# Performance work log

Measured on AMD Instinct MI355X. Metric: run time of the kernel, lower is better.

Reference implementation:

```python
import jax, jax.numpy as jnp
import numpy as np

EPS = 1e-12

def l2_normalize(x, axis=-1):
    # matches torch F.normalize(p=2, dim=1, eps=1e-12) for 2D input
    n = jnp.sqrt(jnp.sum(x * x, axis=axis, keepdims=True))
    return x / jnp.maximum(n, EPS)

def setup_inputs() -> dict:
    key = jax.random.key(0)
    ks = jax.random.split(key, 7)
    N, D = 8192, 256
    s = 1.0 / np.sqrt(D)
    x = jax.random.normal(ks[0], (N, D), dtype=jnp.float32)
    Wq = jax.random.uniform(ks[1], (D, D), jnp.float32, -s, s)
    bq = jax.random.uniform(ks[2], (D,), jnp.float32, -s, s)
    Wk = jax.random.uniform(ks[3], (D, D), jnp.float32, -s, s)
    bk = jax.random.uniform(ks[4], (D,), jnp.float32, -s, s)
    Wv = jax.random.uniform(ks[5], (D, D), jnp.float32, -s, s)
    bv = jax.random.uniform(ks[6], (D,), jnp.float32, -s, s)
    return {"x": x, "Wq": Wq, "bq": bq, "Wk": Wk, "bk": bk, "Wv": Wv, "bv": bv}

def reference(x, Wq, bq, Wk, bk, Wv, bv):
    q = l2_normalize(x @ Wq.T + bq)           # [N, D]
    k = l2_normalize(x @ Wk.T + bk)           # [N, D]
    v = x @ Wv.T + bv                         # [N, D]
    cos_sim = q @ k.T                         # [N, N]
    w = jax.nn.relu(cos_sim)
    # zero diagonal, then renormalize rows to sum 1
    N = w.shape[0]
    w = jnp.where(jnp.eye(N, dtype=bool), 0.0, w)
    w = w / jnp.maximum(jnp.sum(w, axis=-1, keepdims=True), EPS)
    return w @ v + x
```

## Files before the change

kernel.cpp:

```cpp
#include <hip/hip_runtime.h>

#define NROWS 8192
#define DDIM  256
#define KSPLIT 4
#define BM 128
#define BK 64
#define NT (NROWS / KSPLIT / BK)

typedef __bf16 bf16x8 __attribute__((ext_vector_type(8)));
typedef float  f32x4  __attribute__((ext_vector_type(4)));
typedef float  f32x16 __attribute__((ext_vector_type(16)));

typedef __attribute__((address_space(1))) unsigned int uint_gas;
typedef __attribute__((address_space(3))) unsigned int uint_las;

__device__ __forceinline__ void gload_lds16(const void* g, void* l) {
  __builtin_amdgcn_global_load_lds((const uint_gas*)g, (uint_las*)l, 16, 0, 0);
}

__device__ __forceinline__ unsigned int f2bf_bits(float f) {
  union { float f; unsigned int u; } v; v.f = f;
  unsigned int r = v.u + 0x7FFFu + ((v.u >> 16) & 1u);
  return r >> 16;
}
__device__ __forceinline__ float bf2f(unsigned int b) {
  union { unsigned int u; float f; } v; v.u = b << 16;
  return v.f;
}
__device__ __forceinline__ unsigned int pack2bf(float a, float b) {
  union { unsigned int u; __bf16 h[2]; } p;
  p.h[0] = (__bf16)a; p.h[1] = (__bf16)b;
  return p.u;
}
__device__ __forceinline__ unsigned short f2h_bits(float f) {
  union { _Float16 h; unsigned short u; } c; c.h = (_Float16)f;
  return c.u;
}
__device__ __forceinline__ float h2f(unsigned short u) {
  union { unsigned short u; _Float16 h; } c; c.u = u;
  return (float)c.h;
}

#define NXFRAG (512 * 8 * 64)
#define NWFRAG (3 * 16 * 8 * 64)
__global__ __launch_bounds__(256) void convert_kernel(
    const float* __restrict__ x, const float* __restrict__ wq,
    const float* __restrict__ wk, const float* __restrict__ wv,
    unsigned short* __restrict__ xp, unsigned short* __restrict__ Wp)
{
  int tid = blockIdx.x * 256 + threadIdx.x;
  const float* src;
  unsigned short* dst;
  int row, col;
  if (tid < NXFRAG) {
    int l = tid & 63, ks = (tid >> 6) & 7, rt = tid >> 9;
    src = x; dst = xp + (size_t)tid * 8;
    row = rt * 16 + (l & 15); col = ks * 32 + (l >> 4) * 8;
  } else {
    int fid = tid - NXFRAG;
    if (fid >= NWFRAG) return;
    int l = fid & 63, ks = (fid >> 6) & 7, ct = (fid >> 9) & 15, out = fid >> 13;
    src = (out == 0) ? wq : (out == 1) ? wk : wv;
    dst = Wp + (size_t)fid * 8;
    row = ct * 16 + (l & 15); col = ks * 32 + (l >> 4) * 8;
  }
  const float* p = src + (size_t)row * DDIM + col;
  float4 f0 = *(const float4*)p;
  float4 f1 = *(const float4*)(p + 4);
  ushort4 o0, o1;
  o0.x = (unsigned short)f2bf_bits(f0.x); o0.y = (unsigned short)f2bf_bits(f0.y);
  o0.z = (unsigned short)f2bf_bits(f0.z); o0.w = (unsigned short)f2bf_bits(f0.w);
  o1.x = (unsigned short)f2bf_bits(f1.x); o1.y = (unsigned short)f2bf_bits(f1.y);
  o1.z = (unsigned short)f2bf_bits(f1.z); o1.w = (unsigned short)f2bf_bits(f1.w);
  *(ushort4*)dst = o0;
  *(ushort4*)(dst + 4) = o1;
}

__global__ __launch_bounds__(256) void qkv_kernel(
    const float* __restrict__ bq, const float* __restrict__ bk, const float* __restrict__ bv,
    const unsigned short* __restrict__ xp, const unsigned short* __restrict__ Wp,
    unsigned short* __restrict__ qb, unsigned short* __restrict__ kb,
    unsigned short* __restrict__ vT)
{
  __shared__ unsigned short vstage[DDIM * 72];
  const int t = threadIdx.x;
  const int w = t >> 6, l = t & 63;
  const int c = l & 15, g = l >> 4;
  const int out = blockIdx.x / 128;
  const int mb  = blockIdx.x % 128;
  const int row0 = mb * 64;
  const int rw = row0 + w * 16;
  const int rt = mb * 4 + w;

  bf16x8 a[8];
  #pragma unroll
  for (int ks = 0; ks < 8; ks++)
    a[ks] = *(const bf16x8*)(xp + ((size_t)(rt * 8 + ks) * 64 + l) * 8);

  const float* bias = (out == 0) ? bq : (out == 1) ? bk : bv;
  f32x4 vals[16];
  #pragma unroll
  for (int ct = 0; ct < 16; ct++) {
    f32x4 acc = {0.f, 0.f, 0.f, 0.f};
    #pragma unroll
    for (int ks = 0; ks < 8; ks++) {
      bf16x8 b = *(const bf16x8*)(Wp + ((size_t)((out * 16 + ct) * 8 + ks) * 64 + l) * 8);
      acc = __builtin_amdgcn_mfma_f32_16x16x32_bf16(a[ks], b, acc, 0, 0, 0);
    }
    float bias_v = bias[ct * 16 + c];
    #pragma unroll
    for (int r = 0; r < 4; r++) acc[r] += bias_v;
    vals[ct] = acc;
  }
  if (out < 2) {
    #pragma unroll
    for (int r = 0; r < 4; r++) {
      float ss = 0.f;
      #pragma unroll
      for (int ct = 0; ct < 16; ct++) ss += vals[ct][r] * vals[ct][r];
      ss += __shfl_xor(ss, 1); ss += __shfl_xor(ss, 2);
      ss += __shfl_xor(ss, 4); ss += __shfl_xor(ss, 8);
      float inv = 1.f / fmaxf(sqrtf(ss), 1e-12f);
      #pragma unroll
      for (int ct = 0; ct < 16; ct++) vals[ct][r] *= inv;
    }
    unsigned short* dst = (out == 0) ? qb : kb;
    #pragma unroll
    for (int ct = 0; ct < 16; ct++) {
      #pragma unroll
      for (int r = 0; r < 4; r++) {
        unsigned int bits = f2bf_bits(vals[ct][r]);
        unsigned int ob = (unsigned int)__shfl_xor((int)bits, 1);
        if (!(l & 1))
          *(unsigned int*)(dst + (size_t)(rw + g * 4 + r) * DDIM + ct * 16 + c) =
              bits | (ob << 16);
      }
    }
  } else {
    #pragma unroll
    for (int ct = 0; ct < 16; ct++)
      #pragma unroll
      for (int r = 0; r < 4; r++)
        vstage[(ct * 16 + c) * 72 + (w * 16 + g * 4 + r)] =
            (unsigned short)f2bf_bits(vals[ct][r]);
    __syncthreads();
    #pragma unroll
    for (int p = 0; p < 8; p++) {
      int dd = (t >> 3) + p * 32;
      int ch = t & 7;
      *(uint4*)(vT + (size_t)dd * NROWS + row0 + ch * 8) =
          *(const uint4*)(vstage + dd * 72 + ch * 8);
    }
  }
}

__global__ __launch_bounds__(1024, 4) void attn_kernel(
    const unsigned short* __restrict__ qb, const unsigned short* __restrict__ kb,
    const unsigned short* __restrict__ vT,
    unsigned short* __restrict__ nump, float* __restrict__ denp)
{
  __shared__ __align__(16) char smem[163840];
  char* kbuf = smem;
  char* vbuf = smem + 65536;
  char* Pb   = smem + 131072;

  const int t = threadIdx.x;
  const int w = t >> 6, l = t & 63;
  const int l31 = l & 31, hi = l >> 5;
  const int rw = w & 7;
  const int ts = t & 511;
  const int bid = blockIdx.x;
  const int split = bid & (KSPLIT - 1);
  const int mb = bid >> 2;
  const int q0 = mb * BM;
  const int kbase0 = split * (NROWS / KSPLIT);
  const char* kbc = (const char*)kb;
  const char* vtc = (const char*)vT;

  if (w < 8) {
    const int sr = rw >> 1, sc = rw & 1;
    const int qrow = sr * 32 + l31;
    const int qrowg = q0 + qrow;
    const int krl = sc * 32 + l31;
    const int pswz = (qrow & 7) << 4;

    bf16x8 qa[16];
    {
      const unsigned short* qrowp = qb + (size_t)(q0 + qrow) * DDIM + hi * 8;
      #pragma unroll
      for (int m = 0; m < 16; m++) qa[m] = *(const bf16x8*)(qrowp + m * 16);
    }
    float denl = 0.f;

    auto stageK = [&](int buf, int it) {
      const char* ksrc = kbc + (size_t)(kbase0 + it * BK) * 512;
      #pragma unroll
      for (int i = 0; i < 4; i++) {
        int n = i * 512 + ts;
        int row = n >> 5, slot = n & 31;
        gload_lds16(ksrc + row * 512 + (((slot - row) & 31) << 4),
                    kbuf + buf * 32768 + i * 8192 + rw * 1024);
      }
    };

    stageK(0, 0);
    asm volatile("s_waitcnt vmcnt(0)" ::: "memory");
    __builtin_amdgcn_sched_barrier(0);
    __builtin_amdgcn_s_barrier();
    __builtin_amdgcn_sched_barrier(0);

    for (int it = 0; it < NT; ++it) {
      const int cur = it & 1;
      if (it + 1 < NT) stageK(cur ^ 1, it + 1);
      __builtin_amdgcn_sched_barrier(0);

      const char* kcur = kbuf + cur * 32768;
      f32x16 sacc = (f32x16){0.f};
      #pragma unroll
      for (int m = 0; m < 16; m++) {
        bf16x8 kf = *(const bf16x8*)(kcur + krl * 512 +
                                     (((m * 2 + hi + krl) & 31) << 4));
        sacc = __builtin_amdgcn_mfma_f32_32x32x16_bf16(kf, qa[m], sacc, 0, 0, 0);
      }
      char* prowP = Pb + cur * 16384 + qrow * 128;
      const int kbase = kbase0 + it * BK;
      if (__builtin_expect(kbase < q0 + BM && q0 < kbase + BK, 0)) {
        const int dref = qrowg - (kbase + sc * 32 + hi * 4);
        #pragma unroll
        for (int q = 0; q < 4; q++) {
          float v0 = fmaxf(sacc[4 * q + 0], 0.f);
          float v1 = fmaxf(sacc[4 * q + 1], 0.f);
          float v2 = fmaxf(sacc[4 * q + 2], 0.f);
          float v3 = fmaxf(sacc[4 * q + 3], 0.f);
          const int d = dref - 8 * q;
          v0 = (d == 0) ? 0.f : v0;
          v1 = (d == 1) ? 0.f : v1;
          v2 = (d == 2) ? 0.f : v2;
          v3 = (d == 3) ? 0.f : v3;
          denl += (v0 + v1) + (v2 + v3);
          uint2 d2;
          d2.x = pack2bf(v0, v1);
          d2.y = pack2bf(v2, v3);
          *(uint2*)(prowP + ((sc * 64 + q * 16 + hi * 8) ^ pswz)) = d2;
        }
      } else {
        #pragma unroll
        for (int q = 0; q < 4; q++) {
          float v0 = fmaxf(sacc[4 * q + 0], 0.f);
          float v1 = fmaxf(sacc[4 * q + 1], 0.f);
          float v2 = fmaxf(sacc[4 * q + 2], 0.f);
          float v3 = fmaxf(sacc[4 * q + 3], 0.f);
          denl += (v0 + v1) + (v2 + v3);
          uint2 d2;
          d2.x = pack2bf(v0, v1);
          d2.y = pack2bf(v2, v3);
          *(uint2*)(prowP + ((sc * 64 + q * 16 + hi * 8) ^ pswz)) = d2;
        }
      }
      asm volatile("s_waitcnt vmcnt(0) lgkmcnt(0)" ::: "memory");
      __builtin_amdgcn_sched_barrier(0);
      __builtin_amdgcn_s_barrier();
      __builtin_amdgcn_sched_barrier(0);
    }

    float d = denl;
    d += __shfl_xor(d, 32);
    if (l < 32)
      denp[((size_t)split * 2 + sc) * NROWS + q0 + sr * 32 + l] = d;
  } else {
    const int pr = rw >> 2, pc = rw & 3;
    const int pr0 = pr * 64 + l31, pr1 = pr * 64 + 32 + l31;

    f32x16 oacc[2][2];
    #pragma unroll
    for (int rt = 0; rt < 2; rt++)
      #pragma unroll
      for (int dt = 0; dt < 2; dt++)
        oacc[rt][dt] = (f32x16){0.f};

    auto stageV = [&](int buf, int it) {
      const char* vsrc = vtc + (size_t)(kbase0 + it * BK) * 2;
      #pragma unroll
      for (int i = 0; i < 4; i++) {
        int n = i * 512 + ts;
        int dd = n >> 3, slot = n & 7;
        gload_lds16(vsrc + (size_t)dd * (NROWS * 2) + ((slot ^ (dd & 7)) * 16),
                    vbuf + buf * 32768 + i * 8192 + rw * 1024);
      }
    };

    __builtin_amdgcn_s_barrier();
    __builtin_amdgcn_sched_barrier(0);

    for (int it = 0; it < NT; ++it) {
      const int cur = it & 1;
      stageV(cur, it);
      __builtin_amdgcn_sched_barrier(0);

      if (it > 0) {
        const char* Pprev = Pb + (cur ^ 1) * 16384;
        const char* vprev = vbuf + (cur ^ 1) * 32768;
        #pragma unroll
        for (int ch = 0; ch < 4; ch++) {
          const int cb = ch * 32 + hi * 16;
          bf16x8 pa0 = *(const bf16x8*)(Pprev + pr0 * 128 + (cb ^ ((pr0 & 7) << 4)));
          bf16x8 pa1 = *(const bf16x8*)(Pprev + pr1 * 128 + (cb ^ ((pr1 & 7) << 4)));
          #pragma unroll
          for (int dt = 0; dt < 2; dt++) {
            int dl = pc * 64 + dt * 32 + l31;
            bf16x8 vf = *(const bf16x8*)(vprev + dl * 128 + (cb ^ ((dl & 7) << 4)));
            oacc[0][dt] = __builtin_amdgcn_mfma_f32_32x32x16_bf16(pa0, vf, oacc[0][dt], 0, 0, 0);
            oacc[1][dt] = __builtin_amdgcn_mfma_f32_32x32x16_bf16(pa1, vf, oacc[1][dt], 0, 0, 0);
          }
        }
      }
      asm volatile("s_waitcnt vmcnt(0) lgkmcnt(0)" ::: "memory");
      __builtin_amdgcn_sched_barrier(0);
      __builtin_amdgcn_s_barrier();
      __builtin_amdgcn_sched_barrier(0);
    }

    {
      const int last = (NT - 1) & 1;
      const char* Pprev = Pb + last * 16384;
      const char* vprev = vbuf + last * 32768;
      #pragma unroll
      for (int ch = 0; ch < 4; ch++) {
        const int cb = ch * 32 + hi * 16;
        bf16x8 pa0 = *(const bf16x8*)(Pprev + pr0 * 128 + (cb ^ ((pr0 & 7) << 4)));
        bf16x8 pa1 = *(const bf16x8*)(Pprev + pr1 * 128 + (cb ^ ((pr1 & 7) << 4)));
        #pragma unroll
        for (int dt = 0; dt < 2; dt++) {
          int dl = pc * 64 + dt * 32 + l31;
          bf16x8 vf = *(const bf16x8*)(vprev + dl * 128 + (cb ^ ((dl & 7) << 4)));
          oacc[0][dt] = __builtin_amdgcn_mfma_f32_32x32x16_bf16(pa0, vf, oacc[0][dt], 0, 0, 0);
          oacc[1][dt] = __builtin_amdgcn_mfma_f32_32x32x16_bf16(pa1, vf, oacc[1][dt], 0, 0, 0);
        }
      }
    }

    unsigned short* np = nump + (size_t)split * NROWS * DDIM;
    #pragma unroll
    for (int rt = 0; rt < 2; rt++)
      #pragma unroll
      for (int dt = 0; dt < 2; dt++)
        #pragma unroll
        for (int r = 0; r < 16; r++) {
          int rowg = q0 + pr * 64 + rt * 32 + (r & 3) + 8 * (r >> 2) + 4 * hi;
          int col  = pc * 64 + dt * 32 + l31;
          np[(size_t)rowg * DDIM + col] = f2h_bits(oacc[rt][dt][r]);
        }
  }
}

__global__ __launch_bounds__(256) void combine_kernel(
    const float* __restrict__ x,
    const unsigned short* __restrict__ nump, const float* __restrict__ denp,
    float* __restrict__ out)
{
  const int t = threadIdx.x;
  const int w = t >> 6, l = t & 63;
  const int i = blockIdx.x * 4 + w;

  float den = 0.f;
  #pragma unroll
  for (int sp = 0; sp < KSPLIT * 2; sp++)
    den += denp[(size_t)sp * NROWS + i];
  float inv = 1.f / fmaxf(den, 1e-12f);

  const int d0 = l * 4;
  float4 acc = {0.f, 0.f, 0.f, 0.f};
  #pragma unroll
  for (int sp = 0; sp < KSPLIT; sp++) {
    ushort4 u4 = *(const ushort4*)(nump + ((size_t)sp * NROWS + i) * DDIM + d0);
    acc.x += h2f(u4.x); acc.y += h2f(u4.y);
    acc.z += h2f(u4.z); acc.w += h2f(u4.w);
  }
  float4 xx = *(const float4*)(x + (size_t)i * DDIM + d0);
  float4 o;
  o.x = acc.x * inv + xx.x;
  o.y = acc.y * inv + xx.y;
  o.z = acc.z * inv + xx.z;
  o.w = acc.w * inv + xx.w;
  *(float4*)(out + (size_t)i * DDIM + d0) = o;
}

extern "C" void kernel_launch(void* const* d_in, const int* in_sizes, int n_in,
                              void* d_out, int out_size, void* d_ws, size_t ws_size,
                              hipStream_t stream)
{
  const float* x  = (const float*)d_in[0];
  const float* Wq = (const float*)d_in[1];
  const float* bq = (const float*)d_in[2];
  const float* Wk = (const float*)d_in[3];
  const float* bk = (const float*)d_in[4];
  const float* Wv = (const float*)d_in[5];
  const float* bv = (const float*)d_in[6];

  char* ws = (char*)d_ws;
  unsigned short* xp   = (unsigned short*)(ws + 0);
  unsigned short* Wp   = (unsigned short*)(ws + 4194304);
  unsigned short* qb   = (unsigned short*)(ws + 4587520);
  unsigned short* kb   = (unsigned short*)(ws + 8781824);
  unsigned short* vT   = (unsigned short*)(ws + 12976128);
  unsigned short* nump = (unsigned short*)(ws + 17170432);
  float* denp = (float*)(ws + 33947648);

  convert_kernel<<<1120, 256, 0, stream>>>(x, Wq, Wk, Wv, xp, Wp);
  qkv_kernel<<<384, 256, 0, stream>>>(bq, bk, bv, xp, Wp, qb, kb, vT);
  attn_kernel<<<(NROWS / BM) * KSPLIT, 1024, 0, stream>>>(qb, kb, vT, nump, denp);
  combine_kernel<<<NROWS / 4, 256, 0, stream>>>(x, nump, denp, (float*)d_out);
}
```

Measured before the change: 122.6 us.

## Pre-pack V into MFMA fragment tiles and store P in fragment-major layout

The QKV kernel now writes V in a tile-packed layout, with each 64-row block stored as a contiguous 32 KB chunk ordered by MFMA fragment. The attention kernel can then stage V with fully linear 16-byte global-to-LDS loads instead of strided, swizzled loads across 8192-element rows. The P buffer in LDS is also re-laid out as fragment-major 512-byte slabs, which removes the XOR swizzle address math on both the write and read sides. The risk is that the unswizzled layout causes more LDS bank conflicts on the P writes.

```diff
diff --git a/kernel.cpp b/kernel.cpp
--- a/kernel.cpp
+++ b/kernel.cpp
@@ -80,7 +80,7 @@
     const float* __restrict__ bq, const float* __restrict__ bk, const float* __restrict__ bv,
     const unsigned short* __restrict__ xp, const unsigned short* __restrict__ Wp,
     unsigned short* __restrict__ qb, unsigned short* __restrict__ kb,
-    unsigned short* __restrict__ vT)
+    unsigned short* __restrict__ vtp)
 {
   __shared__ unsigned short vstage[DDIM * 72];
   const int t = threadIdx.x;
@@ -144,19 +144,20 @@
         vstage[(ct * 16 + c) * 72 + (w * 16 + g * 4 + r)] =
             (unsigned short)f2bf_bits(vals[ct][r]);
     __syncthreads();
+    unsigned short* wdst = vtp + (size_t)mb * 16384;
     #pragma unroll
     for (int p = 0; p < 8; p++) {
-      int dd = (t >> 3) + p * 32;
-      int ch = t & 7;
-      *(uint4*)(vT + (size_t)dd * NROWS + row0 + ch * 8) =
-          *(const uint4*)(vstage + dd * 72 + ch * 8);
+      int n = p * 256 + t;
+      int dg = ((n >> 8) << 5) + (n & 31);
+      int s  = (n >> 5) & 7;
+      *(uint4*)(wdst + (size_t)n * 8) = *(const uint4*)(vstage + dg * 72 + s * 8);
     }
   }
 }
 
 __global__ __launch_bounds__(1024, 4) void attn_kernel(
     const unsigned short* __restrict__ qb, const unsigned short* __restrict__ kb,
-    const unsigned short* __restrict__ vT,
+    const unsigned short* __restrict__ vtp,
     unsigned short* __restrict__ nump, float* __restrict__ denp)
 {
   __shared__ __align__(16) char smem[163840];
@@ -175,14 +176,13 @@
   const int q0 = mb * BM;
   const int kbase0 = split * (NROWS / KSPLIT);
   const char* kbc = (const char*)kb;
-  const char* vtc = (const char*)vT;
+  const char* vtc = (const char*)vtp;
 
   if (w < 8) {
     const int sr = rw >> 1, sc = rw & 1;
     const int qrow = sr * 32 + l31;
     const int qrowg = q0 + qrow;
     const int krl = sc * 32 + l31;
-    const int pswz = (qrow & 7) << 4;
 
     bf16x8 qa[16];
     {
@@ -222,7 +222,7 @@
                                      (((m * 2 + hi + krl) & 31) << 4));
         sacc = __builtin_amdgcn_mfma_f32_32x32x16_bf16(kf, qa[m], sacc, 0, 0, 0);
       }
-      char* prowP = Pb + cur * 16384 + qrow * 128;
+      char* pbase = Pb + cur * 16384 + sr * 4096 + l31 * 16 + hi * 8;
       const int kbase = kbase0 + it * BK;
       if (__builtin_expect(kbase < q0 + BM && q0 < kbase + BK, 0)) {
         const int dref = qrowg - (kbase + sc * 32 + hi * 4);
@@ -241,7 +241,7 @@
           uint2 d2;
           d2.x = pack2bf(v0, v1);
           d2.y = pack2bf(v2, v3);
-          *(uint2*)(prowP + ((sc * 64 + q * 16 + hi * 8) ^ pswz)) = d2;
+          *(uint2*)(pbase + (sc * 4 + q) * 512) = d2;
         }
       } else {
         #pragma unroll
@@ -254,7 +254,7 @@
           uint2 d2;
           d2.x = pack2bf(v0, v1);
           d2.y = pack2bf(v2, v3);
-          *(uint2*)(prowP + ((sc * 64 + q * 16 + hi * 8) ^ pswz)) = d2;
+          *(uint2*)(pbase + (sc * 4 + q) * 512) = d2;
         }
       }
       asm volatile("s_waitcnt vmcnt(0) lgkmcnt(0)" ::: "memory");
@@ -269,7 +269,6 @@
       denp[((size_t)split * 2 + sc) * NROWS + q0 + sr * 32 + l] = d;
   } else {
     const int pr = rw >> 2, pc = rw & 3;
-    const int pr0 = pr * 64 + l31, pr1 = pr * 64 + 32 + l31;
 
     f32x16 oacc[2][2];
     #pragma unroll
@@ -279,12 +278,11 @@
         oacc[rt][dt] = (f32x16){0.f};
 
     auto stageV = [&](int buf, int it) {
-      const char* vsrc = vtc + (size_t)(kbase0 + it * BK) * 2;
+      const char* vsrc = vtc + (size_t)((kbase0 + it * BK) >> 6) * 32768;
       #pragma unroll
       for (int i = 0; i < 4; i++) {
         int n = i * 512 + ts;
-        int dd = n >> 3, slot = n & 7;
-        gload_lds16(vsrc + (size_t)dd * (NROWS * 2) + ((slot ^ (dd & 7)) * 16),
+        gload_lds16(vsrc + n * 16,
                     vbuf + buf * 32768 + i * 8192 + rw * 1024);
       }
     };
@@ -302,13 +300,12 @@
         const char* vprev = vbuf + (cur ^ 1) * 32768;
         #pragma unroll
         for (int ch = 0; ch < 4; ch++) {
-          const int cb = ch * 32 + hi * 16;
-          bf16x8 pa0 = *(const bf16x8*)(Pprev + pr0 * 128 + (cb ^ ((pr0 & 7) << 4)));
-          bf16x8 pa1 = *(const bf16x8*)(Pprev + pr1 * 128 + (cb ^ ((pr1 & 7) << 4)));
+          const int s512 = (ch * 2 + hi) * 512 + l31 * 16;
+          bf16x8 pa0 = *(const bf16x8*)(Pprev + (pr * 2 + 0) * 4096 + s512);
+          bf16x8 pa1 = *(const bf16x8*)(Pprev + (pr * 2 + 1) * 4096 + s512);
           #pragma unroll
           for (int dt = 0; dt < 2; dt++) {
-            int dl = pc * 64 + dt * 32 + l31;
-            bf16x8 vf = *(const bf16x8*)(vprev + dl * 128 + (cb ^ ((dl & 7) << 4)));
+            bf16x8 vf = *(const bf16x8*)(vprev + (pc * 2 + dt) * 4096 + s512);
             oacc[0][dt] = __builtin_amdgcn_mfma_f32_32x32x16_bf16(pa0, vf, oacc[0][dt], 0, 0, 0);
             oacc[1][dt] = __builtin_amdgcn_mfma_f32_32x32x16_bf16(pa1, vf, oacc[1][dt], 0, 0, 0);
           }
@@ -326,13 +323,12 @@
       const char* vprev = vbuf + last * 32768;
       #pragma unroll
       for (int ch = 0; ch < 4; ch++) {
-        const int cb = ch * 32 + hi * 16;
-        bf16x8 pa0 = *(const bf16x8*)(Pprev + pr0 * 128 + (cb ^ ((pr0 & 7) << 4)));
-        bf16x8 pa1 = *(const bf16x8*)(Pprev + pr1 * 128 + (cb ^ ((pr1 & 7) << 4)));
+        const int s512 = (ch * 2 + hi) * 512 + l31 * 16;
+        bf16x8 pa0 = *(const bf16x8*)(Pprev + (pr * 2 + 0) * 4096 + s512);
+        bf16x8 pa1 = *(const bf16x8*)(Pprev + (pr * 2 + 1) * 4096 + s512);
         #pragma unroll
         for (int dt = 0; dt < 2; dt++) {
-          int dl = pc * 64 + dt * 32 + l31;
-          bf16x8 vf = *(const bf16x8*)(vprev + dl * 128 + (cb ^ ((dl & 7) << 4)));
+          bf16x8 vf = *(const bf16x8*)(vprev + (pc * 2 + dt) * 4096 + s512);
           oacc[0][dt] = __builtin_amdgcn_mfma_f32_32x32x16_bf16(pa0, vf, oacc[0][dt], 0, 0, 0);
           oacc[1][dt] = __builtin_amdgcn_mfma_f32_32x32x16_bf16(pa1, vf, oacc[1][dt], 0, 0, 0);
         }
@@ -402,12 +398,12 @@
   unsigned short* Wp   = (unsigned short*)(ws + 4194304);
   unsigned short* qb   = (unsigned short*)(ws + 4587520);
   unsigned short* kb   = (unsigned short*)(ws + 8781824);
-  unsigned short* vT   = (unsigned short*)(ws + 12976128);
+  unsigned short* vtp  = (unsigned short*)(ws + 12976128);
   unsigned short* nump = (unsigned short*)(ws + 17170432);
   float* denp = (float*)(ws + 33947648);
 
   convert_kernel<<<1120, 256, 0, stream>>>(x, Wq, Wk, Wv, xp, Wp);
-  qkv_kernel<<<384, 256, 0, stream>>>(bq, bk, bv, xp, Wp, qb, kb, vT);
-  attn_kernel<<<(NROWS / BM) * KSPLIT, 1024, 0, stream>>>(qb, kb, vT, nump, denp);
+  qkv_kernel<<<384, 256, 0, stream>>>(bq, bk, bv, xp, Wp, qb, kb, vtp);
+  attn_kernel<<<(NROWS / BM) * KSPLIT, 1024, 0, stream>>>(qb, kb, vtp, nump, denp);
   combine_kernel<<<NROWS / 4, 256, 0, stream>>>(x, nump, denp, (float*)d_out);
 }
```

Result: no change. 122.0 us (-0.5%).
